# Kernel optimization log

Measured on AMD Instinct MI355X. Metric: run time of the kernel, lower is better.

Reference implementation:

```python
import jax, jax.numpy as jnp
import numpy as np

NOPEN = 64
NNIN = 16
NUM_OUTPUT = 64
NLAYER = 4
H = 0.1
TF = 1.0
N_NODES = 50000
N_EDGES = 1600000


def setup_inputs() -> dict:
    key = jax.random.key(0)
    k1, k2, k3, k4, k5, k6 = jax.random.split(key, 6)
    xn = jax.random.normal(k1, (1, NNIN, N_NODES), dtype=jnp.float32)
    iInd = jax.random.randint(k2, (N_EDGES,), 0, N_NODES)
    jInd = jax.random.randint(k3, (N_EDGES,), 0, N_NODES)
    # learned parameters per original init
    K1Nopen = jax.random.normal(k4, (NOPEN, NNIN), dtype=jnp.float32) * 0.01
    KN1 = jnp.eye(NOPEN, dtype=jnp.float32) + jax.random.uniform(k5, (NOPEN, NOPEN), dtype=jnp.float32) * 0.001
    KNclose = jax.random.normal(k6, (NUM_OUTPUT, NOPEN), dtype=jnp.float32) * 0.01
    return {"xn": xn, "iInd": iInd, "jInd": jInd, "n_nodes": N_NODES,
            "K1Nopen": K1Nopen, "KN1": KN1, "KNclose": KNclose}


def _gcn_norm(I, J, n_nodes, dtype):
    # add self-loops, symmetric normalization deg^{-1/2}[row]*deg^{-1/2}[col]
    loops = jnp.arange(n_nodes, dtype=I.dtype)
    I2 = jnp.concatenate([I, loops])
    J2 = jnp.concatenate([J, loops])
    ew = jnp.ones(I2.shape[0], dtype=dtype)
    deg = jax.ops.segment_sum(ew, J2, num_segments=n_nodes)
    dinv = jnp.where(deg > 0, 1.0 / jnp.sqrt(deg), 0.0)
    w = dinv[I2] * dinv[J2]
    return I2, J2, w


def reference(xn, iInd, jInd, n_nodes, K1Nopen, KN1, KNclose):
    I, J, w = _gcn_norm(iInd, jInd, n_nodes, xn.dtype)  # [E+N]

    # OpenFlatLayer: 1x1 conv1d with K1Nopen + relu (openclose=True, norm=False)
    x = jax.nn.relu(jnp.einsum('oi,bin->bon', K1Nopen, xn))  # [1, nopen, N]

    dt = TF / NLAYER
    wb = w[None, None, :]
    for _ in range(NLAYER):
        # nodeGrad: edge features [1, nopen, E]
        g = wb * (x[:, :, I] - x[:, :, J])
        # singleLayer (openclose=False): conv(K), relu, conv(K.t())
        z = jax.nn.relu(jnp.einsum('oi,bie->boe', KN1, g))
        z = jnp.einsum('io,bie->boe', KN1, z)
        # edgeDiv: scatter-add w*z at I minus at J
        wz = jnp.moveaxis(wb * z, -1, 0)  # [E, 1, nopen]
        div = (jax.ops.segment_sum(wz, I, num_segments=n_nodes)
               - jax.ops.segment_sum(wz, J, num_segments=n_nodes))
        div = jnp.moveaxis(div, 0, -1)  # [1, nopen, N]
        # forward Euler: step layer returns -h*div, integrated with dt
        x = x - dt * H * div

    # CloseLayer: 1x1 conv1d, squeeze().t(), log_softmax over channels
    xc = jnp.einsum('oi,bin->bon', KNclose, x)[0].T  # [N, num_output]
    return jax.nn.log_softmax(xc, axis=1)
```

## Files before the change

### kernel.cpp

```cpp
#include <hip/hip_runtime.h>

#define NN 50000
#define NE 1600000
#define C 64
#define NIN 16
#define DTH 0.025f
#define ASC 16.0f
#define USC 64.0f
#define SDIV 16384.0f
#define SLOT 128

#define NB2 256
#define NPB 196
#define CAP 16384
#define ABLK 1024
#define EPB 1563
#define RND 2048
#define BINC 32
#define GSTR 16

typedef _Float16 f16x2 __attribute__((ext_vector_type(2)));
typedef float f32x2 __attribute__((ext_vector_type(2)));
union U32H2 { uint32_t u; f16x2 h; };

#define RL(x, l) __int_as_float(__builtin_amdgcn_readlane(__float_as_int(x), (l)))

__global__ void k_setup(const float* __restrict__ KN1, const float* __restrict__ KNc,
                        float* __restrict__ M2s, float* __restrict__ KMs,
                        int* __restrict__ gcur) {
    if (threadIdx.x < NB2) gcur[threadIdx.x * GSTR] = 0;
    for (int idx = threadIdx.x; idx < C * C; idx += blockDim.x) {
        int p = idx >> 6, o = idx & 63;
        float s1 = 0.f, s2 = 0.f;
        for (int i = 0; i < C; i++) {
            s1 = fmaf(KN1[o * C + i], KN1[p * C + i], s1);
            s2 = fmaf(KNc[o * C + i], KN1[p * C + i], s2);
        }
        M2s[idx] = s1;
        KMs[idx] = s2;
    }
}

static __device__ __forceinline__ void store_u8(uint32_t* __restrict__ u8, int n, int lane, float su) {
    float v1 = __shfl_down(su, 1, 64);
    float v2 = __shfl_down(su, 2, 64);
    float v3 = __shfl_down(su, 3, 64);
    if ((lane & 3) == 0) {
        int p0 = __builtin_amdgcn_cvt_pk_fp8_f32(su, v1, 0, false);
        int p1 = __builtin_amdgcn_cvt_pk_fp8_f32(v2, v3, p0, true);
        u8[n * 16 + (lane >> 2)] = (uint32_t)p1;
    }
}

__launch_bounds__(512)
__global__ void k_binA_open(const int* __restrict__ iInd, const int* __restrict__ jInd,
                            int* __restrict__ gcur, uint32_t* __restrict__ stg,
                            const float* __restrict__ xn, const float* __restrict__ K1,
                            const float* __restrict__ KN1, const float* __restrict__ KNc,
                            _Float16* __restrict__ u0, uint32_t* __restrict__ u8,
                            float* __restrict__ co) {
    __shared__ __align__(16) char smem[36864];
    __shared__ int bcnt[NB2];
    __shared__ int gbase[NB2];
    __shared__ float sxn[NIN][17];
    uint32_t (*bins)[BINC] = (uint32_t(*)[BINC])smem;
    int tid = threadIdx.x;
    int eBeg = blockIdx.x * EPB;
    int eEnd = eBeg + EPB; if (eEnd > NE) eEnd = NE;
    for (int rb = eBeg; rb < eEnd; rb += RND) {
        for (int b = tid; b < NB2; b += 512) bcnt[b] = 0;
        __syncthreads();
        int rEnd = rb + RND; if (rEnd > eEnd) rEnd = eEnd;
        for (int e = rb + tid; e < rEnd; e += 512) {
            int i = __builtin_nontemporal_load(&iInd[e]);
            int j = __builtin_nontemporal_load(&jInd[e]);
            {
                int b = (unsigned)i / NPB;
                uint32_t ent = ((unsigned)(i - b * NPB) << 17) | (unsigned)j;
                int pos = atomicAdd(&bcnt[b], 1);
                if (pos < BINC) bins[b][pos] = ent;
                else { int gp = atomicAdd(&gcur[b * GSTR], 1);
                       if (gp < CAP) stg[(size_t)b * CAP + gp] = ent; }
            }
            {
                int b = (unsigned)j / NPB;
                uint32_t ent = ((unsigned)(j - b * NPB) << 17) | 0x10000u | (unsigned)i;
                int pos = atomicAdd(&bcnt[b], 1);
                if (pos < BINC) bins[b][pos] = ent;
                else { int gp = atomicAdd(&gcur[b * GSTR], 1);
                       if (gp < CAP) stg[(size_t)b * CAP + gp] = ent; }
            }
        }
        __syncthreads();
        if (tid < NB2) {
            int c = bcnt[tid]; if (c > BINC) c = BINC;
            gbase[tid] = (c > 0) ? atomicAdd(&gcur[tid * GSTR], c) : 0;
        }
        __syncthreads();
        for (int idx = tid; idx < NB2 * BINC; idx += 512) {
            int b = idx >> 5, k = idx & (BINC - 1);
            int c = bcnt[b]; if (c > BINC) c = BINC;
            if (k < c) {
                int pos = gbase[b] + k;
                if (pos < CAP) stg[(size_t)b * CAP + pos] = bins[b][k];
            }
        }
        __syncthreads();
    }
    float* sK1 = (float*)smem;
    float* sU  = sK1 + NIN * C;
    float* sC  = sU + C * C;
    for (int idx = tid; idx < NIN * C; idx += 512) {
        int i = idx >> 6, o = idx & 63;
        sK1[idx] = K1[o * NIN + i];
    }
    for (int idx = tid; idx < C * C; idx += 512) {
        int o = idx >> 6, p = idx & 63;
        int sw = (o << 6) | (p ^ ((o & 7) << 2));
        sU[sw] = KN1[idx];
        sC[sw] = KNc[idx];
    }
    int wv = tid >> 6, lane = tid & 63;
    int mb = lane << 6, lx = (lane & 7) << 2;
    int w2 = wv * 2;
    int nit = 3 + (blockIdx.x < 53 ? 1 : 0);
    int fi = tid >> 4, ft = tid & 15;
    float vpre = 0.f;
    if (tid < 256) vpre = xn[fi * NN + blockIdx.x * 16 + ft];
    for (int it = 0; it < nit; it++) {
        __syncthreads();
        if (tid < 256) sxn[fi][ft] = vpre;
        __syncthreads();
        if (it + 1 < nit && tid < 256)
            vpre = xn[fi * NN + blockIdx.x * 16 + (it + 1) * 16384 + ft];
        int pr = blockIdx.x * 8 + wv + it * 8192;
        int nA = pr * 2, nB = nA + 1;
        float xA = 0.f, xB = 0.f;
#pragma unroll
        for (int i = 0; i < NIN; i++) {
            float k1 = sK1[i * C + lane];
            xA = fmaf(k1, sxn[i][w2], xA);
            xB = fmaf(k1, sxn[i][w2 + 1], xB);
        }
        xA = fmaxf(xA, 0.f); xB = fmaxf(xB, 0.f);
        float uA0 = 0.f, uA1 = 0.f, uB0 = 0.f, uB1 = 0.f;
        float cA0 = 0.f, cA1 = 0.f, cB0 = 0.f, cB1 = 0.f;
#pragma unroll
        for (int p0 = 0; p0 < C; p0 += 4) {
            const float4 mu = *(const float4*)&sU[mb + (p0 ^ lx)];
            const float4 mc = *(const float4*)&sC[mb + (p0 ^ lx)];
            float a0 = RL(xA, p0 + 0), a1 = RL(xA, p0 + 1);
            float a2 = RL(xA, p0 + 2), a3 = RL(xA, p0 + 3);
            float b0 = RL(xB, p0 + 0), b1 = RL(xB, p0 + 1);
            float b2 = RL(xB, p0 + 2), b3 = RL(xB, p0 + 3);
            uA0 = fmaf(mu.x, a0, uA0); uA1 = fmaf(mu.y, a1, uA1);
            uA0 = fmaf(mu.z, a2, uA0); uA1 = fmaf(mu.w, a3, uA1);
            uB0 = fmaf(mu.x, b0, uB0); uB1 = fmaf(mu.y, b1, uB1);
            uB0 = fmaf(mu.z, b2, uB0); uB1 = fmaf(mu.w, b3, uB1);
            cA0 = fmaf(mc.x, a0, cA0); cA1 = fmaf(mc.y, a1, cA1);
            cA0 = fmaf(mc.z, a2, cA0); cA1 = fmaf(mc.w, a3, cA1);
            cB0 = fmaf(mc.x, b0, cB0); cB1 = fmaf(mc.y, b1, cB1);
            cB0 = fmaf(mc.z, b2, cB0); cB1 = fmaf(mc.w, b3, cB1);
        }
        float uA = uA0 + uA1, uB = uB0 + uB1;
        u0[(size_t)nA * C + lane] = (_Float16)uA;
        u0[(size_t)nB * C + lane] = (_Float16)uB;
        store_u8(u8, nA, lane, uA * USC);
        store_u8(u8, nB, lane, uB * USC);
        co[(size_t)nA * C + lane] = cA0 + cA1;
        co[(size_t)nB * C + lane] = cB0 + cB1;
    }
}

#define LADJ (NPB * SLOT)
__launch_bounds__(1024)
__global__ void k_binB(const int* __restrict__ gcur, const uint32_t* __restrict__ stg,
                       unsigned* __restrict__ pk, float* __restrict__ dinv,
                       uint32_t* __restrict__ adjp) {
    __shared__ unsigned lcnt[NPB];
    __shared__ uint32_t ladj[LADJ];
    int b = blockIdx.x, tid = threadIdx.x;
    if (tid < NPB) lcnt[tid] = 0;
    __syncthreads();
    int cnt = gcur[b * GSTR]; if (cnt > CAP) cnt = CAP;
    int n0 = b * NPB;
    for (int k = tid; k < cnt; k += 1024) {
        uint32_t ent = stg[(size_t)b * CAP + k];
        int tl = (int)(ent >> 17);
        unsigned sign = (ent >> 16) & 1u;
        unsigned other = ent & 0xFFFFu;
        unsigned ret = atomicAdd(&lcnt[tl], 1u + (sign << 16));
        unsigned slot = ret & 0xFFFFu;
        if (slot < SLOT) ladj[(tl << 7) + slot] = other | (sign << 31);
    }
    __syncthreads();
    if (tid < NPB) {
        int n = n0 + tid;
        if (n < NN) {
            unsigned v = lcnt[tid];
            unsigned c = v & 0xFFFFu; if (c > SLOT) c = SLOT;
            unsigned deg = (v >> 16) + 1u;
            pk[n] = (deg << 16) | c;
            dinv[n] = 1.0f / sqrtf((float)deg);
        }
    }
    int nval = NN - n0; if (nval > NPB) nval = NPB; if (nval < 0) nval = 0;
    int totv = (nval << 7) >> 2;
    uint4* gdst = (uint4*)(adjp + ((size_t)n0 << 7));
    const uint4* lsrc = (const uint4*)ladj;
    for (int v = tid; v < totv; v += 1024) gdst[v] = lsrc[v];
}

__global__ void k_weight(const unsigned* __restrict__ pk, const float* __restrict__ dinv,
                         uint32_t* __restrict__ adjp) {
    int idx = blockIdx.x * 256 + threadIdx.x;
    int n = idx >> 7, p = idx & (SLOT - 1);
    int cnt = (int)(pk[n] & 0xFFFFu); if (cnt > SLOT) cnt = SLOT;
    int pad = (cnt + 31) & ~31;
    if (p < cnt) {
        uint32_t e = adjp[idx];
        int other = (int)(e & 0xFFFFu);
        float a = ASC * dinv[n] * dinv[other];
        if (e >> 31) a = -a;
        U32H2 t; t.u = (unsigned)other; t.h.y = (_Float16)a;
        adjp[idx] = t.u;
    } else if (p < pad) {
        adjp[idx] = 0u;
    }
}

#define ACCR(WW, QQ, A01, A23, U01, U23) {                                    \
    U32H2 aw; aw.u = (WW);                                                    \
    float a_ = (float)aw.h.y;                                                 \
    f32x2 av_; av_.x = a_; av_.y = a_;                                        \
    f32x2 lo_ = __builtin_amdgcn_cvt_pk_f32_fp8((int)(QQ), false);            \
    f32x2 hi_ = __builtin_amdgcn_cvt_pk_f32_fp8((int)(QQ), true);             \
    f32x2 t01_ = av_ * ((U01) - lo_);                                         \
    f32x2 t23_ = av_ * ((U23) - hi_);                                         \
    t01_ = __builtin_elementwise_max(t01_, zz);                               \
    t23_ = __builtin_elementwise_max(t23_, zz);                               \
    A01 = av_ * t01_ + A01;                                                   \
    A23 = av_ * t23_ + A23;                                                   \
}

#define GATHER2_BODY(PKA, ADJP, U8R)                                          \
    uint32_t unqA = (U8R)[nA * 16 + li];                                      \
    uint32_t unqB = (U8R)[nB * 16 + li];                                      \
    f32x2 uA01 = __builtin_amdgcn_cvt_pk_f32_fp8((int)unqA, false);           \
    f32x2 uA23 = __builtin_amdgcn_cvt_pk_f32_fp8((int)unqA, true);            \
    f32x2 uB01 = __builtin_amdgcn_cvt_pk_f32_fp8((int)unqB, false);           \
    f32x2 uB23 = __builtin_amdgcn_cvt_pk_f32_fp8((int)unqB, true);            \
    uint2 pk2_ = *(const uint2*)&(PKA)[nA];                                   \
    int degA = (int)(pk2_.x & 0xFFFFu); if (degA > SLOT) degA = SLOT;         \
    int degB = (int)(pk2_.y & 0xFFFFu); if (degB > SLOT) degB = SLOT;         \
    int padA = (degA + 31) & ~31, padB = (degB + 31) & ~31;                   \
    int baseA = nA << 7, baseB = nB << 7;                                     \
    int maxPad = padA > padB ? padA : padB;                                   \
    f32x2 zz; zz.x = 0.f; zz.y = 0.f;                                         \
    f32x2 aA01 = zz, aA23 = zz, aB01 = zz, aB23 = zz;                         \
    uint32_t wA[8], wB[8];                                                    \
    if (padA > 0) {                                                           \
        _Pragma("unroll")                                                     \
        for (int r = 0; r < 8; r++) wA[r] = (ADJP)[baseA + r * 4 + g];        \
    }                                                                         \
    if (padB > 0) {                                                           \
        _Pragma("unroll")                                                     \
        for (int r = 0; r < 8; r++) wB[r] = (ADJP)[baseB + r * 4 + g];        \
    }                                                                         \
    for (int c0 = 0; c0 < maxPad; c0 += 32) {                                 \
        uint32_t qA[8], qB[8], wA2[8], wB2[8];                                \
        bool dA = c0 < padA, dB = c0 < padB;                                  \
        bool dA2 = c0 + 32 < padA, dB2 = c0 + 32 < padB;                      \
        if (dA) {                                                             \
            _Pragma("unroll")                                                 \
            for (int r = 0; r < 8; r++) qA[r] = (U8R)[(wA[r] & 0xFFFFu) * 16 + li]; \
        }                                                                     \
        if (dB) {                                                             \
            _Pragma("unroll")                                                 \
            for (int r = 0; r < 8; r++) qB[r] = (U8R)[(wB[r] & 0xFFFFu) * 16 + li]; \
        }                                                                     \
        if (dA2) {                                                            \
            _Pragma("unroll")                                                 \
            for (int r = 0; r < 8; r++) wA2[r] = (ADJP)[baseA + c0 + 32 + r * 4 + g]; \
        }                                                                     \
        if (dB2) {                                                            \
            _Pragma("unroll")                                                 \
            for (int r = 0; r < 8; r++) wB2[r] = (ADJP)[baseB + c0 + 32 + r * 4 + g]; \
        }                                                                     \
        if (dA) {                                                             \
            _Pragma("unroll")                                                 \
            for (int r = 0; r < 8; r++) ACCR(wA[r], qA[r], aA01, aA23, uA01, uA23) \
        }                                                                     \
        if (dB) {                                                             \
            _Pragma("unroll")                                                 \
            for (int r = 0; r < 8; r++) ACCR(wB[r], qB[r], aB01, aB23, uB01, uB23) \
        }                                                                     \
        if (dA2) {                                                            \
            _Pragma("unroll")                                                 \
            for (int r = 0; r < 8; r++) wA[r] = wA2[r];                       \
        }                                                                     \
        if (dB2) {                                                            \
            _Pragma("unroll")                                                 \
            for (int r = 0; r < 8; r++) wB[r] = wB2[r];                       \
        }                                                                     \
    }                                                                         \
    float aA0 = aA01.x, aA1 = aA01.y, aA2 = aA23.x, aA3 = aA23.y;             \
    float aB0 = aB01.x, aB1 = aB01.y, aB2 = aB23.x, aB3 = aB23.y;             \
    aA0 += __shfl_xor(aA0, 16, 64); aA0 += __shfl_xor(aA0, 32, 64);           \
    aA1 += __shfl_xor(aA1, 16, 64); aA1 += __shfl_xor(aA1, 32, 64);           \
    aA2 += __shfl_xor(aA2, 16, 64); aA2 += __shfl_xor(aA2, 32, 64);           \
    aA3 += __shfl_xor(aA3, 16, 64); aA3 += __shfl_xor(aA3, 32, 64);           \
    aB0 += __shfl_xor(aB0, 16, 64); aB0 += __shfl_xor(aB0, 32, 64);           \
    aB1 += __shfl_xor(aB1, 16, 64); aB1 += __shfl_xor(aB1, 32, 64);           \
    aB2 += __shfl_xor(aB2, 16, 64); aB2 += __shfl_xor(aB2, 32, 64);           \
    aB3 += __shfl_xor(aB3, 16, 64); aB3 += __shfl_xor(aB3, 32, 64);           \
    float rA0 = __shfl(aA0, lane >> 2, 64), rA1 = __shfl(aA1, lane >> 2, 64); \
    float rA2 = __shfl(aA2, lane >> 2, 64), rA3 = __shfl(aA3, lane >> 2, 64); \
    float rB0 = __shfl(aB0, lane >> 2, 64), rB1 = __shfl(aB1, lane >> 2, 64); \
    float rB2 = __shfl(aB2, lane >> 2, 64), rB3 = __shfl(aB3, lane >> 2, 64); \
    float sA_lane = (lane & 2) ? ((lane & 1) ? rA3 : rA2)                     \
                               : ((lane & 1) ? rA1 : rA0);                    \
    float sB_lane = (lane & 2) ? ((lane & 1) ? rB3 : rB2)                     \
                               : ((lane & 1) ? rB1 : rB0);

#define STAGE_MT(SMT, SRC) {                                                  \
    for (int idx = threadIdx.x; idx < C * C; idx += 256) {                    \
        int p_ = idx >> 6, c_ = idx & 63;                                     \
        (SMT)[(c_ << 6) | (p_ ^ ((c_ & 7) << 2))] = (SRC)[idx];               \
    }                                                                         \
}

#define MATVEC2(SMT, SAV, SBV, DUA, DUB) {                                    \
    float mA0_ = 0.f, mA1_ = 0.f, mB0_ = 0.f, mB1_ = 0.f;                     \
    int mb_ = (lane << 6), lx_ = (lane & 7) << 2;                             \
    _Pragma("unroll")                                                         \
    for (int p0 = 0; p0 < 64; p0 += 4) {                                      \
        const float4 mv = *(const float4*)&(SMT)[mb_ + (p0 ^ lx_)];           \
        mA0_ = fmaf(mv.x, RL(SAV, p0 + 0), mA0_);                             \
        mA1_ = fmaf(mv.y, RL(SAV, p0 + 1), mA1_);                             \
        mA0_ = fmaf(mv.z, RL(SAV, p0 + 2), mA0_);                             \
        mA1_ = fmaf(mv.w, RL(SAV, p0 + 3), mA1_);                             \
        mB0_ = fmaf(mv.x, RL(SBV, p0 + 0), mB0_);                             \
        mB1_ = fmaf(mv.y, RL(SBV, p0 + 1), mB1_);                             \
        mB0_ = fmaf(mv.z, RL(SBV, p0 + 2), mB0_);                             \
        mB1_ = fmaf(mv.w, RL(SBV, p0 + 3), mB1_);                             \
    }                                                                         \
    DUA = mA0_ + mA1_; DUB = mB0_ + mB1_;                                     \
}

__launch_bounds__(256, 6)
__global__ void k_gather_upd(const unsigned* __restrict__ pk, const uint32_t* __restrict__ adjp,
                             const uint32_t* __restrict__ u8r, const _Float16* __restrict__ ucur,
                             const float* __restrict__ M2s, float* __restrict__ sacc,
                             _Float16* __restrict__ unext, uint32_t* __restrict__ u8w, int beta) {
    __shared__ float sMt[C * C];
    STAGE_MT(sMt, M2s)
    __syncthreads();
    int wv = threadIdx.x >> 6, lane = threadIdx.x & 63;
    int g = lane >> 4, li = lane & 15;
    int nA = (blockIdx.x * 4 + wv) * 2;
    int nB = nA + 1;
    GATHER2_BODY(pk, adjp, u8r)
    float duA, duB;
    MATVEC2(sMt, sA_lane, sB_lane, duA, duB)
    float unewA = (float)ucur[(size_t)nA * C + lane] - (DTH / SDIV) * duA;
    float unewB = (float)ucur[(size_t)nB * C + lane] - (DTH / SDIV) * duB;
    unext[(size_t)nA * C + lane] = (_Float16)unewA;
    unext[(size_t)nB * C + lane] = (_Float16)unewB;
    store_u8(u8w, nA, lane, unewA * USC);
    store_u8(u8w, nB, lane, unewB * USC);
    size_t ixA = (size_t)nA * C + lane, ixB = (size_t)nB * C + lane;
    sacc[ixA] = beta ? (sacc[ixA] + sA_lane) : sA_lane;
    sacc[ixB] = beta ? (sacc[ixB] + sB_lane) : sB_lane;
}

__launch_bounds__(256, 6)
__global__ void k_gather_close(const unsigned* __restrict__ pk, const uint32_t* __restrict__ adjp,
                               const uint32_t* __restrict__ u8r, const float* __restrict__ KMs,
                               const float* __restrict__ sacc, const float* __restrict__ co,
                               float* __restrict__ out) {
    __shared__ float sKMt[C * C];
    STAGE_MT(sKMt, KMs)
    __syncthreads();
    int wv = threadIdx.x >> 6, lane = threadIdx.x & 63;
    int g = lane >> 4, li = lane & 15;
    int nA = (blockIdx.x * 4 + wv) * 2;
    int nB = nA + 1;
    GATHER2_BODY(pk, adjp, u8r)
    float stotA = sA_lane + sacc[(size_t)nA * C + lane];
    float stotB = sB_lane + sacc[(size_t)nB * C + lane];
    float dxA, dxB;
    MATVEC2(sKMt, stotA, stotB, dxA, dxB)
    float oA = co[(size_t)nA * C + lane] - (DTH / SDIV) * dxA;
    float oB = co[(size_t)nB * C + lane] - (DTH / SDIV) * dxB;
    float mA = oA, mB = oB;
#pragma unroll
    for (int off2 = 32; off2; off2 >>= 1) {
        mA = fmaxf(mA, __shfl_xor(mA, off2, 64));
        mB = fmaxf(mB, __shfl_xor(mB, off2, 64));
    }
    float sumA = expf(oA - mA), sumB = expf(oB - mB);
#pragma unroll
    for (int off2 = 32; off2; off2 >>= 1) {
        sumA += __shfl_xor(sumA, off2, 64);
        sumB += __shfl_xor(sumB, off2, 64);
    }
    out[(size_t)nA * C + lane] = oA - mA - logf(sumA);
    out[(size_t)nB * C + lane] = oB - mB - logf(sumB);
}

extern "C" void kernel_launch(void* const* d_in, const int* in_sizes, int n_in,
                              void* d_out, int out_size, void* d_ws, size_t ws_size,
                              hipStream_t stream) {
    (void)in_sizes; (void)n_in; (void)out_size; (void)ws_size;
    const float* xn   = (const float*)d_in[0];
    const int* iInd   = (const int*)d_in[1];
    const int* jInd   = (const int*)d_in[2];
    const float* K1   = (const float*)d_in[4];
    const float* KN1  = (const float*)d_in[5];
    const float* KNc  = (const float*)d_in[6];
    float* out = (float*)d_out;

    char* base = (char*)d_ws;
    size_t off = 0;
    auto alloc = [&](size_t bytes) { char* p = base + off; off = (off + bytes + 255) & ~(size_t)255; return p; };
    float* M2s  = (float*)alloc(C * C * 4);
    float* KMs  = (float*)alloc(C * C * 4);
    int* gcur   = (int*)alloc(NB2 * GSTR * 4);
    unsigned* pk = (unsigned*)alloc(NN * 4);
    float* dinv = (float*)alloc(NN * 4);
    float* co   = (float*)alloc((size_t)NN * C * 4);
    float* sacc = (float*)alloc((size_t)NN * C * 4);
    _Float16* ua = (_Float16*)alloc((size_t)NN * C * 2);
    _Float16* ub = (_Float16*)alloc((size_t)NN * C * 2);
    uint32_t* u8a = (uint32_t*)alloc((size_t)NN * 16 * 4);
    uint32_t* u8b = (uint32_t*)alloc((size_t)NN * 16 * 4);
    uint32_t* stg = (uint32_t*)alloc((size_t)NB2 * CAP * 4);
    uint32_t* adjp = (uint32_t*)alloc((size_t)NN * SLOT * 4);

    k_setup<<<1, 256, 0, stream>>>(KN1, KNc, M2s, KMs, gcur);
    k_binA_open<<<ABLK, 512, 0, stream>>>(iInd, jInd, gcur, stg, xn, K1, KN1, KNc, ua, u8a, co);
    k_binB<<<NB2, 1024, 0, stream>>>(gcur, stg, pk, dinv, adjp);
    k_weight<<<(NN * SLOT) / 256, 256, 0, stream>>>(pk, dinv, adjp);

    const int GB = NN / 8;
    k_gather_upd<<<GB, 256, 0, stream>>>(pk, adjp, u8a, ua, M2s, sacc, ub, u8b, 0);
    k_gather_upd<<<GB, 256, 0, stream>>>(pk, adjp, u8b, ub, M2s, sacc, ua, u8a, 1);
    k_gather_upd<<<GB, 256, 0, stream>>>(pk, adjp, u8a, ua, M2s, sacc, ub, u8b, 1);
    k_gather_close<<<GB, 256, 0, stream>>>(pk, adjp, u8b, KMs, sacc, co, out);
}
```

Before: 460.7 us.

## Hold matvec weights in registers instead of LDS and drop adjacency prefetch

Removes the per-block LDS staging of the 64x64 matrix, along with its barrier, in both gather kernels. Each lane now loads its matrix column into 64 registers straight from global memory, and launch bounds drop from 6 to 4 blocks per CU to make room. Separately, the software double-buffered prefetch of adjacency words is removed: each chunk loads its adjacency indices and then the dependent gathers. This trades LDS traffic and staging cost for higher register pressure, lower occupancy, and less latency hiding in the gather loop.

```diff
diff --git a/kernel.cpp b/kernel.cpp
--- a/kernel.cpp
+++ b/kernel.cpp
@@ -258,35 +258,25 @@
     int maxPad = padA > padB ? padA : padB;                                   \
     f32x2 zz; zz.x = 0.f; zz.y = 0.f;                                         \
     f32x2 aA01 = zz, aA23 = zz, aB01 = zz, aB23 = zz;                         \
-    uint32_t wA[8], wB[8];                                                    \
-    if (padA > 0) {                                                           \
-        _Pragma("unroll")                                                     \
-        for (int r = 0; r < 8; r++) wA[r] = (ADJP)[baseA + r * 4 + g];        \
-    }                                                                         \
-    if (padB > 0) {                                                           \
-        _Pragma("unroll")                                                     \
-        for (int r = 0; r < 8; r++) wB[r] = (ADJP)[baseB + r * 4 + g];        \
-    }                                                                         \
     for (int c0 = 0; c0 < maxPad; c0 += 32) {                                 \
-        uint32_t qA[8], qB[8], wA2[8], wB2[8];                                \
+        uint32_t wA[8], qA[8], wB[8], qB[8];                                  \
         bool dA = c0 < padA, dB = c0 < padB;                                  \
-        bool dA2 = c0 + 32 < padA, dB2 = c0 + 32 < padB;                      \
         if (dA) {                                                             \
             _Pragma("unroll")                                                 \
+            for (int r = 0; r < 8; r++) wA[r] = (ADJP)[baseA + c0 + r * 4 + g]; \
+        }                                                                     \
+        if (dB) {                                                             \
+            _Pragma("unroll")                                                 \
+            for (int r = 0; r < 8; r++) wB[r] = (ADJP)[baseB + c0 + r * 4 + g]; \
+        }                                                                     \
+        if (dA) {                                                             \
+            _Pragma("unroll")                                                 \
             for (int r = 0; r < 8; r++) qA[r] = (U8R)[(wA[r] & 0xFFFFu) * 16 + li]; \
         }                                                                     \
         if (dB) {                                                             \
             _Pragma("unroll")                                                 \
             for (int r = 0; r < 8; r++) qB[r] = (U8R)[(wB[r] & 0xFFFFu) * 16 + li]; \
         }                                                                     \
-        if (dA2) {                                                            \
-            _Pragma("unroll")                                                 \
-            for (int r = 0; r < 8; r++) wA2[r] = (ADJP)[baseA + c0 + 32 + r * 4 + g]; \
-        }                                                                     \
-        if (dB2) {                                                            \
-            _Pragma("unroll")                                                 \
-            for (int r = 0; r < 8; r++) wB2[r] = (ADJP)[baseB + c0 + 32 + r * 4 + g]; \
-        }                                                                     \
         if (dA) {                                                             \
             _Pragma("unroll")                                                 \
             for (int r = 0; r < 8; r++) ACCR(wA[r], qA[r], aA01, aA23, uA01, uA23) \
@@ -294,14 +284,6 @@
         if (dB) {                                                             \
             _Pragma("unroll")                                                 \
             for (int r = 0; r < 8; r++) ACCR(wB[r], qB[r], aB01, aB23, uB01, uB23) \
-        }                                                                     \
-        if (dA2) {                                                            \
-            _Pragma("unroll")                                                 \
-            for (int r = 0; r < 8; r++) wA[r] = wA2[r];                       \
-        }                                                                     \
-        if (dB2) {                                                            \
-            _Pragma("unroll")                                                 \
-            for (int r = 0; r < 8; r++) wB[r] = wB2[r];                       \
         }                                                                     \
     }                                                                         \
     float aA0 = aA01.x, aA1 = aA01.y, aA2 = aA23.x, aA3 = aA23.y;             \
@@ -323,46 +305,35 @@
     float sB_lane = (lane & 2) ? ((lane & 1) ? rB3 : rB2)                     \
                                : ((lane & 1) ? rB1 : rB0);
 
-#define STAGE_MT(SMT, SRC) {                                                  \
-    for (int idx = threadIdx.x; idx < C * C; idx += 256) {                    \
-        int p_ = idx >> 6, c_ = idx & 63;                                     \
-        (SMT)[(c_ << 6) | (p_ ^ ((c_ & 7) << 2))] = (SRC)[idx];               \
+#define MATVEC2R(VM, SAV, SBV, DUA, DUB) {                                    \
+    float dA0_ = 0.f, dA1_ = 0.f, dB0_ = 0.f, dB1_ = 0.f;                     \
+    _Pragma("unroll")                                                         \
+    for (int p0 = 0; p0 < C; p0 += 2) {                                       \
+        float sa0_ = RL(SAV, p0), sa1_ = RL(SAV, p0 + 1);                     \
+        float sb0_ = RL(SBV, p0), sb1_ = RL(SBV, p0 + 1);                     \
+        dA0_ = fmaf((VM)[p0], sa0_, dA0_);                                    \
+        dA1_ = fmaf((VM)[p0 + 1], sa1_, dA1_);                                \
+        dB0_ = fmaf((VM)[p0], sb0_, dB0_);                                    \
+        dB1_ = fmaf((VM)[p0 + 1], sb1_, dB1_);                                \
     }                                                                         \
-}
-
-#define MATVEC2(SMT, SAV, SBV, DUA, DUB) {                                    \
-    float mA0_ = 0.f, mA1_ = 0.f, mB0_ = 0.f, mB1_ = 0.f;                     \
-    int mb_ = (lane << 6), lx_ = (lane & 7) << 2;                             \
-    _Pragma("unroll")                                                         \
-    for (int p0 = 0; p0 < 64; p0 += 4) {                                      \
-        const float4 mv = *(const float4*)&(SMT)[mb_ + (p0 ^ lx_)];           \
-        mA0_ = fmaf(mv.x, RL(SAV, p0 + 0), mA0_);                             \
-        mA1_ = fmaf(mv.y, RL(SAV, p0 + 1), mA1_);                             \
-        mA0_ = fmaf(mv.z, RL(SAV, p0 + 2), mA0_);                             \
-        mA1_ = fmaf(mv.w, RL(SAV, p0 + 3), mA1_);                             \
-        mB0_ = fmaf(mv.x, RL(SBV, p0 + 0), mB0_);                             \
-        mB1_ = fmaf(mv.y, RL(SBV, p0 + 1), mB1_);                             \
-        mB0_ = fmaf(mv.z, RL(SBV, p0 + 2), mB0_);                             \
-        mB1_ = fmaf(mv.w, RL(SBV, p0 + 3), mB1_);                             \
-    }                                                                         \
-    DUA = mA0_ + mA1_; DUB = mB0_ + mB1_;                                     \
-}
-
-__launch_bounds__(256, 6)
+    DUA = dA0_ + dA1_; DUB = dB0_ + dB1_;                                     \
+}
+
+__launch_bounds__(256, 4)
 __global__ void k_gather_upd(const unsigned* __restrict__ pk, const uint32_t* __restrict__ adjp,
                              const uint32_t* __restrict__ u8r, const _Float16* __restrict__ ucur,
                              const float* __restrict__ M2s, float* __restrict__ sacc,
                              _Float16* __restrict__ unext, uint32_t* __restrict__ u8w, int beta) {
-    __shared__ float sMt[C * C];
-    STAGE_MT(sMt, M2s)
-    __syncthreads();
     int wv = threadIdx.x >> 6, lane = threadIdx.x & 63;
     int g = lane >> 4, li = lane & 15;
+    float vM[C];
+#pragma unroll
+    for (int p = 0; p < C; p++) vM[p] = M2s[p * C + lane];
     int nA = (blockIdx.x * 4 + wv) * 2;
     int nB = nA + 1;
     GATHER2_BODY(pk, adjp, u8r)
     float duA, duB;
-    MATVEC2(sMt, sA_lane, sB_lane, duA, duB)
+    MATVEC2R(vM, sA_lane, sB_lane, duA, duB)
     float unewA = (float)ucur[(size_t)nA * C + lane] - (DTH / SDIV) * duA;
     float unewB = (float)ucur[(size_t)nB * C + lane] - (DTH / SDIV) * duB;
     unext[(size_t)nA * C + lane] = (_Float16)unewA;
@@ -374,23 +345,23 @@
     sacc[ixB] = beta ? (sacc[ixB] + sB_lane) : sB_lane;
 }
 
-__launch_bounds__(256, 6)
+__launch_bounds__(256, 4)
 __global__ void k_gather_close(const unsigned* __restrict__ pk, const uint32_t* __restrict__ adjp,
                                const uint32_t* __restrict__ u8r, const float* __restrict__ KMs,
                                const float* __restrict__ sacc, const float* __restrict__ co,
                                float* __restrict__ out) {
-    __shared__ float sKMt[C * C];
-    STAGE_MT(sKMt, KMs)
-    __syncthreads();
     int wv = threadIdx.x >> 6, lane = threadIdx.x & 63;
     int g = lane >> 4, li = lane & 15;
+    float vM[C];
+#pragma unroll
+    for (int p = 0; p < C; p++) vM[p] = KMs[p * C + lane];
     int nA = (blockIdx.x * 4 + wv) * 2;
     int nB = nA + 1;
     GATHER2_BODY(pk, adjp, u8r)
     float stotA = sA_lane + sacc[(size_t)nA * C + lane];
     float stotB = sB_lane + sacc[(size_t)nB * C + lane];
     float dxA, dxB;
-    MATVEC2(sKMt, stotA, stotB, dxA, dxB)
+    MATVEC2R(vM, stotA, stotB, dxA, dxB)
     float oA = co[(size_t)nA * C + lane] - (DTH / SDIV) * dxA;
     float oB = co[(size_t)nB * C + lane] - (DTH / SDIV) * dxB;
     float mA = oA, mB = oB;
```

Result: slower. 484.7 us (+5.2%).
